# Kernel optimization log

Measured on AMD Instinct MI355X. Metric: run time of the kernel, lower is better.

## Reference

```python
import jax, jax.numpy as jnp
import numpy as np

B, T = 4, 8192
C = 64            # dilation_channels (also embedding size)
S = 256           # skip_dims
V = 256           # waveform_categories (8-bit mu-law)
CENTER = 128      # waveform_center_cat
DILATIONS = [1, 2, 4, 8, 16, 32, 64, 128, 256, 512] * 3  # 3 blocks, 30 layers
L = len(DILATIONS)


def setup_inputs() -> dict:
    key = jax.random.key(0)
    ks = jax.random.split(key, 16)
    waveform = jax.random.randint(ks[0], (B, T, 1), 0, V, dtype=jnp.int32)
    waveform_lens = jax.random.randint(ks[1], (B,), 0, T, dtype=jnp.int32)
    s = 0.05
    embed = jax.random.normal(ks[2], (V, C), dtype=jnp.float32) * s
    # conv_w[l, 0] applies to x[t-d], conv_w[l, 1] to x[t] (kernel_size=2)
    conv_w = jax.random.normal(ks[3], (L, 2, C, 2 * C), dtype=jnp.float32) * s
    conv_b = jnp.zeros((L, 2 * C), dtype=jnp.float32)
    res_w = jax.random.normal(ks[4], (L, C, C), dtype=jnp.float32) * s
    res_b = jnp.zeros((L, C), dtype=jnp.float32)
    skip_w = jax.random.normal(ks[5], (L, C, S), dtype=jnp.float32) * s
    skip_b = jnp.zeros((L, S), dtype=jnp.float32)
    w0 = jax.random.normal(ks[6], (S, V), dtype=jnp.float32) * s
    b0 = jnp.zeros((V,), dtype=jnp.float32)
    w1 = jax.random.normal(ks[7], (V, V), dtype=jnp.float32) * s
    b1 = jnp.zeros((V,), dtype=jnp.float32)
    return dict(waveform=waveform, waveform_lens=waveform_lens, embed=embed,
                conv_w=conv_w, conv_b=conv_b, res_w=res_w, res_b=res_b,
                skip_w=skip_w, skip_b=skip_b, w0=w0, b0=b0, w1=w1, b1=b1)


def _wavenet(wf, lens, embed, conv_w, conv_b, res_w, res_b, skip_w, skip_b, w0, b0, w1, b1):
    labels = wf[..., 0]                                          # (B, T) int
    # shift right with <go> = center category
    inp = jnp.concatenate(
        [jnp.full((B, 1), CENTER, dtype=labels.dtype), labels[:, :-1]], axis=1)
    x = embed[inp]                                               # (B, T, C)
    skip_sum = jnp.zeros((B, T, S), dtype=x.dtype)
    for i, d in enumerate(DILATIONS):
        # dilated causal conv, kernel 2: y[t] = x[t-d] @ W0 + x[t] @ W1 + b
        x_shift = jnp.pad(x, ((0, 0), (d, 0), (0, 0)))[:, :T]    # left pad d
        h = (jnp.einsum('btc,cf->btf', x_shift, conv_w[i, 0])
             + jnp.einsum('btc,cf->btf', x, conv_w[i, 1]) + conv_b[i])
        gate = jnp.tanh(h[..., :C]) * jax.nn.sigmoid(h[..., C:])  # (B, T, C)
        x = x + jnp.einsum('btc,cd->btd', gate, res_w[i]) + res_b[i]
        skip_sum = skip_sum + jnp.einsum('btc,cs->bts', gate, skip_w[i]) + skip_b[i]
    hid0 = jax.nn.relu(jnp.einsum('bts,sv->btv', skip_sum, w0) + b0)
    logits = jnp.einsum('btv,vu->btu', hid0, w1) + b1            # (B, T, V)
    logp = jax.nn.log_softmax(logits, axis=-1)
    ce = -jnp.take_along_axis(logp, labels[..., None], axis=-1)[..., 0]  # (B, T)
    mask = (jnp.arange(T)[None, :] < lens[:, None]).astype(logits.dtype)
    loss = jnp.sum(ce * mask) / jnp.maximum(jnp.sum(mask), 1.0)
    return loss


def reference(waveform, waveform_lens, embed, conv_w, conv_b, res_w, res_b,
              skip_w, skip_b, w0, b0, w1, b1):
    return _wavenet(waveform, waveform_lens, embed, conv_w, conv_b, res_w,
                    res_b, skip_w, skip_b, w0, b0, w1, b1)
```

## Files before the change

kernel.cpp:

```cpp
#include <hip/hip_runtime.h>

#define NB 4
#define NT 8192
#define NC 64
#define NS 256
#define NV 256
#define NL 30

typedef __attribute__((ext_vector_type(8))) short bf16x8;
typedef __attribute__((ext_vector_type(4))) float f32x4;
typedef unsigned short ushort_t;

#define MFMA(a, b, c) __builtin_amdgcn_mfma_f32_16x16x32_bf16(a, b, c, 0, 0, 0)

#define OFF_WCAT 0
#define SZ_WCAT  (NL * 16384)
#define OFF_RW   (OFF_WCAT + SZ_WCAT)
#define SZ_RW    (NL * 4096)
#define OFF_SWG  (OFF_RW + SZ_RW)
#define SZ_SWG   (6 * 81920)
#define OFF_W0   (OFF_SWG + SZ_SWG)
#define OFF_W1   (OFF_W0 + 65536)
#define TOTAL_W  (OFF_W1 + 65536)
#define N_PREP   (TOTAL_W + 1792)

#define X_ELEMS  (NB * NT * NC)
#define SK_ELEMS (NB * NT * NS)
#define G_ELEMS  (NB * NT * NC)

#define WS_SMALL ((size_t)(2 * X_ELEMS + SK_ELEMS + 5 * G_ELEMS + TOTAL_W) * 2 \
                  + 1792 * 4)
#define WS_BIG   ((size_t)(2 * X_ELEMS + 30 * G_ELEMS + TOTAL_W) * 2 + 1792 * 4)

__device__ inline ushort_t f2bu(float f) {
  union { float f; unsigned u; } v; v.f = f;
  unsigned r = v.u + 0x7FFFu + ((v.u >> 16) & 1u);
  return (ushort_t)(r >> 16);
}
__device__ inline float b2f(ushort_t h) {
  union { unsigned u; float f; } v; v.u = ((unsigned)h) << 16; return v.f;
}

__global__ void sentinel_kernel(float* __restrict__ out) {
  if (threadIdx.x == 0) out[0] = -1234.0f;
}

__global__ __launch_bounds__(256) void prep_kernel(
    const float* __restrict__ cw, const float* __restrict__ rw,
    const float* __restrict__ sw, const float* __restrict__ w0,
    const float* __restrict__ w1, const float* __restrict__ sb_all,
    ushort_t* __restrict__ wt, float* __restrict__ sbg,
    float* __restrict__ out0)
{
  int idx = blockIdx.x * 256 + threadIdx.x;
  if (idx == 0) out0[0] = 0.f;
  if (idx >= N_PREP) return;
  if (idx >= TOTAL_W) {
    int j = idx - TOTAL_W;
    if (j < 1536) {
      int g = j >> 8, n = j & 255;
      float s = 0.f;
#pragma unroll
      for (int jj = 0; jj < 5; ++jj) s += sb_all[(5 * g + jj) * 256 + n];
      sbg[j] = s;
    } else {
      int n = j - 1536;
      float s = 0.f;
      for (int jj = 0; jj < NL; ++jj) s += sb_all[jj * 256 + n];
      sbg[j] = s;
    }
    return;
  }
  float v;
  if (idx < OFF_RW) {
    int e = idx; int l = e >> 14; int r = e & 16383;
    int kk = r >> 12, n = (r >> 5) & 127, j = r & 31;
    int k = kk * 32 + j, tap = k >> 6, c = k & 63;
    v = cw[(((l * 2 + tap) << 6) + c) * 128 + n];
  } else if (idx < OFF_SWG) {
    int e = idx - OFF_RW; int l = e >> 12; int r = e & 4095;
    int kk = r >> 11, n = (r >> 5) & 63, j = r & 31;
    int k = kk * 32 + j;
    v = rw[((l << 6) + k) * 64 + n];
  } else if (idx < OFF_W0) {
    int e = idx - OFF_SWG; int g = e / 81920; int r = e % 81920;
    int kk = r >> 13; int rem = r & 8191;
    int n = rem >> 5, jj = rem & 31;
    int k = kk * 32 + jj;
    v = sw[(size_t)(320 * g + k) * 256 + n];
  } else if (idx < OFF_W1) {
    int e = idx - OFF_W0;
    int kk = e >> 13; int rem = e & 8191;
    int n = rem >> 5, jj = rem & 31;
    int k = kk * 32 + jj;
    v = w0[k * 256 + n];
  } else {
    int e = idx - OFF_W1;
    int kk = e >> 13; int rem = e & 8191;
    int n = rem >> 5, jj = rem & 31;
    int k = kk * 32 + jj;
    v = w1[k * 256 + n];
  }
  wt[idx] = f2bu(v);
}

__global__ __launch_bounds__(256) void embed_kernel(
    const int* __restrict__ wf, const float* __restrict__ embed,
    ushort_t* __restrict__ x0)
{
  const int bidx = blockIdx.x;
  const int bb = bidx >> 7;
  const int t0 = (bidx & 127) << 6;
  const int pos0 = bb * NT + t0;
  for (int e = threadIdx.x; e < 64 * 64; e += 256) {
    int p = e >> 6, c = e & 63;
    int t = t0 + p;
    int id = (t == 0) ? 128 : wf[bb * NT + t - 1];
    x0[(size_t)(pos0 + p) * NC + c] = f2bu(embed[id * NC + c]);
  }
}

__global__ __launch_bounds__(384) void chain5_kernel(
    const ushort_t* __restrict__ xin, ushort_t* __restrict__ xout,
    ushort_t* __restrict__ gates,
    const ushort_t* __restrict__ wt,
    const float* __restrict__ cb_all, const float* __restrict__ rb_all,
    int l0, const int* __restrict__ wf, const float* __restrict__ embf)
{
  __shared__ __align__(16) ushort_t xt[96][72];
  __shared__ __align__(16) ushort_t gt[96][72];

  const int tid = threadIdx.x;
  const int w = tid >> 6, lane = tid & 63;
  const int quad = lane >> 4, c16 = lane & 15;
  const int bb = blockIdx.x >> 7;
  const int t0 = (blockIdx.x & 127) << 6;
  const size_t row0 = (size_t)bb * NT;

#pragma unroll
  for (int i = 0; i < 2; ++i) {
    int e = tid + i * 384;
    int r = e >> 3, c0 = (e & 7) * 8;
    int t = t0 - 32 + r;
    bf16x8 v;
    if (t >= 0) {
      if (embf) {
        int id = (t == 0) ? 128 : wf[row0 + t - 1];
        const float* ep = embf + id * NC + c0;
#pragma unroll
        for (int jj = 0; jj < 8; ++jj) v[jj] = (short)f2bu(ep[jj]);
      } else {
        v = *(const bf16x8*)(xin + (row0 + t) * 64 + c0);
      }
    } else { bf16x8 z = {0, 0, 0, 0, 0, 0, 0, 0}; v = z; }
    *(bf16x8*)&xt[r][c0] = v;
  }
  __syncthreads();

  for (int j = 0; j < 5; ++j) {
    const int l = l0 + j;
    const int d = 1 << j;
    const ushort_t* wcat = wt + OFF_WCAT + l * 16384;
    const ushort_t* rww  = wt + OFF_RW + l * 4096;
    const float* cb = cb_all + l * 128;
    const float* rb = rb_all + l * 64;

    bf16x8 af[4];
    {
      int lr = w * 16 + c16;
#pragma unroll
      for (int kk = 0; kk < 4; ++kk) {
        int rr = (kk < 2) ? lr - d : lr;
        int ch = (kk & 1) * 32 + quad * 8;
        if (rr >= 0) af[kk] = *(const bf16x8*)&xt[rr][ch];
        else { bf16x8 z = {0, 0, 0, 0, 0, 0, 0, 0}; af[kk] = z; }
      }
    }
    __syncthreads();

    {
      f32x4 acc[8];
#pragma unroll
      for (int q = 0; q < 4; ++q) {
        float ba = cb[q * 16 + c16], bs = cb[q * 16 + c16 + 64];
        f32x4 va = {ba, ba, ba, ba}, vb = {bs, bs, bs, bs};
        acc[q] = va; acc[4 + q] = vb;
      }
#pragma unroll
      for (int kk = 0; kk < 4; ++kk) {
        const ushort_t* wp = wcat + kk * 4096 + c16 * 32 + quad * 8;
#pragma unroll
        for (int q = 0; q < 4; ++q) {
          acc[q]     = MFMA(af[kk], *(const bf16x8*)(wp + q * 512), acc[q]);
          acc[4 + q] = MFMA(af[kk], *(const bf16x8*)(wp + q * 512 + 2048), acc[4 + q]);
        }
      }
#pragma unroll
      for (int q = 0; q < 4; ++q)
#pragma unroll
        for (int r = 0; r < 4; ++r) {
          float e2 = __expf(2.f * acc[q][r]);
          float th = (e2 - 1.f) / (e2 + 1.f);
          float sg = 1.f / (1.f + __expf(-acc[4 + q][r]));
          gt[w * 16 + quad * 4 + r][q * 16 + c16] = f2bu(th * sg);
        }

      bf16x8 gf0 = *(const bf16x8*)&gt[w * 16 + c16][quad * 8];
      bf16x8 gf1 = *(const bf16x8*)&gt[w * 16 + c16][32 + quad * 8];

      f32x4 acc2[4];
#pragma unroll
      for (int q = 0; q < 4; ++q) {
        float bv = rb[q * 16 + c16];
        f32x4 z = {bv, bv, bv, bv};
        acc2[q] = z;
      }
      const ushort_t* wp2 = rww + c16 * 32 + quad * 8;
#pragma unroll
      for (int q = 0; q < 4; ++q)
        acc2[q] = MFMA(gf0, *(const bf16x8*)(wp2 + q * 512), acc2[q]);
#pragma unroll
      for (int q = 0; q < 4; ++q)
        acc2[q] = MFMA(gf1, *(const bf16x8*)(wp2 + q * 512 + 2048), acc2[q]);
#pragma unroll
      for (int q = 0; q < 4; ++q) {
        int n = q * 16 + c16;
#pragma unroll
        for (int r = 0; r < 4; ++r) {
          int rowi = w * 16 + quad * 4 + r;
          xt[rowi][n] = f2bu(b2f(xt[rowi][n]) + acc2[q][r]);
        }
      }
    }
    __syncthreads();

    {
      ushort_t* gslot = gates + (size_t)j * G_ELEMS;
      int e = tid;
      {
        int r = e >> 3, c0 = (e & 7) * 8;
        *(bf16x8*)(gslot + (row0 + t0 + r) * 64 + c0) =
            *(const bf16x8*)&gt[32 + r][c0];
      }
      e = tid + 384;
      if (e < 512) {
        int r = e >> 3, c0 = (e & 7) * 8;
        *(bf16x8*)(gslot + (row0 + t0 + r) * 64 + c0) =
            *(const bf16x8*)&gt[32 + r][c0];
      }
    }
  }
  __syncthreads();

  {
    int e = tid;
    {
      int r = e >> 3, c0 = (e & 7) * 8;
      *(bf16x8*)(xout + (row0 + t0 + r) * 64 + c0) = *(const bf16x8*)&xt[32 + r][c0];
    }
    e = tid + 384;
    if (e < 512) {
      int r = e >> 3, c0 = (e & 7) * 8;
      *(bf16x8*)(xout + (row0 + t0 + r) * 64 + c0) = *(const bf16x8*)&xt[32 + r][c0];
    }
  }
}

__global__ __launch_bounds__(384) void chain5hi_kernel(
    const ushort_t* __restrict__ xin, ushort_t* __restrict__ xout,
    ushort_t* __restrict__ gates,
    const ushort_t* __restrict__ wt,
    const float* __restrict__ cb_all, const float* __restrict__ rb_all,
    int lbase, int write_x)
{
  __shared__ __align__(16) ushort_t xt[96][72];
  __shared__ __align__(16) ushort_t gt[96][72];

  const int tid = threadIdx.x;
  const int w = tid >> 6, lane = tid & 63;
  const int quad = lane >> 4, c16 = lane & 15;
  const int bb = blockIdx.x >> 7;
  const int sub = blockIdx.x & 127;
  const int k = sub & 31;
  const int i0 = (sub >> 5) << 6;
  const size_t row0 = (size_t)bb * NT;

#pragma unroll
  for (int i = 0; i < 2; ++i) {
    int e = tid + i * 384;
    int r = e >> 3, c0 = (e & 7) * 8;
    int ii = i0 + r - 32;
    bf16x8 v;
    if (ii >= 0) v = *(const bf16x8*)(xin + (row0 + (size_t)ii * 32 + k) * 64 + c0);
    else { bf16x8 z = {0, 0, 0, 0, 0, 0, 0, 0}; v = z; }
    *(bf16x8*)&xt[r][c0] = v;
  }
  __syncthreads();

  for (int j = 0; j < 5; ++j) {
    const int l = lbase + j;
    const int d = 1 << j;
    const ushort_t* wcat = wt + OFF_WCAT + l * 16384;
    const ushort_t* rww  = wt + OFF_RW + l * 4096;
    const float* cb = cb_all + l * 128;
    const float* rb = rb_all + l * 64;

    bf16x8 af[4];
    {
      int lr = w * 16 + c16;
#pragma unroll
      for (int kk = 0; kk < 4; ++kk) {
        int rr = (kk < 2) ? lr - d : lr;
        int ch = (kk & 1) * 32 + quad * 8;
        if (rr >= 0) af[kk] = *(const bf16x8*)&xt[rr][ch];
        else { bf16x8 z = {0, 0, 0, 0, 0, 0, 0, 0}; af[kk] = z; }
      }
    }
    __syncthreads();

    {
      f32x4 acc[8];
#pragma unroll
      for (int q = 0; q < 4; ++q) {
        float ba = cb[q * 16 + c16], bs = cb[q * 16 + c16 + 64];
        f32x4 va = {ba, ba, ba, ba}, vb = {bs, bs, bs, bs};
        acc[q] = va; acc[4 + q] = vb;
      }
#pragma unroll
      for (int kk = 0; kk < 4; ++kk) {
        const ushort_t* wp = wcat + kk * 4096 + c16 * 32 + quad * 8;
#pragma unroll
        for (int q = 0; q < 4; ++q) {
          acc[q]     = MFMA(af[kk], *(const bf16x8*)(wp + q * 512), acc[q]);
          acc[4 + q] = MFMA(af[kk], *(const bf16x8*)(wp + q * 512 + 2048), acc[4 + q]);
        }
      }
#pragma unroll
      for (int q = 0; q < 4; ++q)
#pragma unroll
        for (int r = 0; r < 4; ++r) {
          float e2 = __expf(2.f * acc[q][r]);
          float th = (e2 - 1.f) / (e2 + 1.f);
          float sg = 1.f / (1.f + __expf(-acc[4 + q][r]));
          gt[w * 16 + quad * 4 + r][q * 16 + c16] = f2bu(th * sg);
        }

      if (write_x || j < 4) {
        bf16x8 gf0 = *(const bf16x8*)&gt[w * 16 + c16][quad * 8];
        bf16x8 gf1 = *(const bf16x8*)&gt[w * 16 + c16][32 + quad * 8];

        f32x4 acc2[4];
#pragma unroll
        for (int q = 0; q < 4; ++q) {
          float bv = rb[q * 16 + c16];
          f32x4 z = {bv, bv, bv, bv};
          acc2[q] = z;
        }
        const ushort_t* wp2 = rww + c16 * 32 + quad * 8;
#pragma unroll
        for (int q = 0; q < 4; ++q)
          acc2[q] = MFMA(gf0, *(const bf16x8*)(wp2 + q * 512), acc2[q]);
#pragma unroll
        for (int q = 0; q < 4; ++q)
          acc2[q] = MFMA(gf1, *(const bf16x8*)(wp2 + q * 512 + 2048), acc2[q]);
#pragma unroll
        for (int q = 0; q < 4; ++q) {
          int n = q * 16 + c16;
#pragma unroll
          for (int r = 0; r < 4; ++r) {
            int rowi = w * 16 + quad * 4 + r;
            xt[rowi][n] = f2bu(b2f(xt[rowi][n]) + acc2[q][r]);
          }
        }
      }
    }
    __syncthreads();

    {
      ushort_t* gslot = gates + (size_t)j * G_ELEMS;
      int e = tid;
      {
        int r = e >> 3, c0 = (e & 7) * 8;
        *(bf16x8*)(gslot + (row0 + (size_t)(i0 + r) * 32 + k) * 64 + c0) =
            *(const bf16x8*)&gt[32 + r][c0];
      }
      e = tid + 384;
      if (e < 512) {
        int r = e >> 3, c0 = (e & 7) * 8;
        *(bf16x8*)(gslot + (row0 + (size_t)(i0 + r) * 32 + k) * 64 + c0) =
            *(const bf16x8*)&gt[32 + r][c0];
      }
    }
  }
  __syncthreads();

  if (write_x) {
    int e = tid;
    {
      int r = e >> 3, c0 = (e & 7) * 8;
      *(bf16x8*)(xout + (row0 + (size_t)(i0 + r) * 32 + k) * 64 + c0) =
          *(const bf16x8*)&xt[32 + r][c0];
    }
    e = tid + 384;
    if (e < 512) {
      int r = e >> 3, c0 = (e & 7) * 8;
      *(bf16x8*)(xout + (row0 + (size_t)(i0 + r) * 32 + k) * 64 + c0) =
          *(const bf16x8*)&xt[32 + r][c0];
    }
  }
}

__global__ __launch_bounds__(256) void skip30_head_kernel(
    const ushort_t* __restrict__ gates,
    const ushort_t* __restrict__ wt,
    const float* __restrict__ sbtot,
    const float* __restrict__ b0, const float* __restrict__ b1,
    const int* __restrict__ wf, const int* __restrict__ lens,
    float* __restrict__ loss)
{
  __shared__ __align__(16) ushort_t wbuf[2][8192];
  __shared__ __align__(16) ushort_t tile[64][264];
  const int tid = threadIdx.x;
  const int w = tid >> 6, lane = tid & 63;
  const int quad = lane >> 4, c16 = lane & 15;
  const int bb = blockIdx.x >> 7;
  const int t0 = (blockIdx.x & 127) << 6;
  const int tb = t0 + w * 16;
  const size_t row0 = (size_t)bb * NT;
  const int mylen = lens[bb];
  const ushort_t* swg = wt + OFF_SWG;

  f32x4 acc[16];
#pragma unroll
  for (int nt = 0; nt < 16; ++nt) { f32x4 z = {0.f, 0.f, 0.f, 0.f}; acc[nt] = z; }

  const size_t arow = (row0 + tb + c16) * 64;
  bf16x8 wreg[4];
#pragma unroll
  for (int i = 0; i < 4; ++i)
    wreg[i] = ((const bf16x8*)swg)[tid + i * 256];
  bf16x8 af = *(const bf16x8*)(gates + arow + quad * 8);
  int cur = 0;

  for (int kk = 0; kk < 60; ++kk) {
#pragma unroll
    for (int i = 0; i < 4; ++i)
      ((bf16x8*)wbuf[cur])[tid + i * 256] = wreg[i];
    int kn = (kk + 1 < 60) ? kk + 1 : 59;
#pragma unroll
    for (int i = 0; i < 4; ++i)
      wreg[i] = ((const bf16x8*)(swg + (size_t)kn * 8192))[tid + i * 256];
    bf16x8 afn = *(const bf16x8*)(gates + (size_t)(kn >> 1) * G_ELEMS + arow +
                                  (kn & 1) * 32 + quad * 8);
    __syncthreads();
    const ushort_t* wp = wbuf[cur] + c16 * 32 + quad * 8;
#pragma unroll
    for (int nt = 0; nt < 16; ++nt)
      acc[nt] = MFMA(af, *(const bf16x8*)(wp + nt * 512), acc[nt]);
    af = afn; cur ^= 1;
  }

#pragma unroll
  for (int nt = 0; nt < 16; ++nt) {
    int n = nt * 16 + c16;
    float sbn = sbtot[n];
#pragma unroll
    for (int r = 0; r < 4; ++r)
      tile[w * 16 + quad * 4 + r][n] = f2bu(acc[nt][r] + sbn);
  }

  const ushort_t* w0T = wt + OFF_W0;
  f32x4 accA[16];
#pragma unroll
  for (int nt = 0; nt < 16; ++nt) {
    float bv = b0[nt * 16 + c16];
    f32x4 z = {bv, bv, bv, bv};
    accA[nt] = z;
  }
  for (int kk = 0; kk < 8; ++kk) {
#pragma unroll
    for (int i = 0; i < 4; ++i)
      ((bf16x8*)wbuf[0])[tid + i * 256] = ((const bf16x8*)(w0T + kk * 8192))[tid + i * 256];
    __syncthreads();
    bf16x8 hf = *(const bf16x8*)&tile[w * 16 + c16][kk * 32 + quad * 8];
    const ushort_t* wp = wbuf[0] + c16 * 32 + quad * 8;
#pragma unroll
    for (int nt = 0; nt < 16; ++nt)
      accA[nt] = MFMA(hf, *(const bf16x8*)(wp + nt * 512), accA[nt]);
    __syncthreads();
  }
#pragma unroll
  for (int nt = 0; nt < 16; ++nt)
#pragma unroll
    for (int r = 0; r < 4; ++r)
      tile[w * 16 + quad * 4 + r][nt * 16 + c16] = f2bu(fmaxf(accA[nt][r], 0.f));

  const ushort_t* w1T = wt + OFF_W1;
  f32x4 acc2[16];
#pragma unroll
  for (int nt = 0; nt < 16; ++nt) {
    float bv = b1[nt * 16 + c16];
    f32x4 z = {bv, bv, bv, bv};
    acc2[nt] = z;
  }
  for (int kk = 0; kk < 8; ++kk) {
#pragma unroll
    for (int i = 0; i < 4; ++i)
      ((bf16x8*)wbuf[0])[tid + i * 256] = ((const bf16x8*)(w1T + kk * 8192))[tid + i * 256];
    __syncthreads();
    bf16x8 hf = *(const bf16x8*)&tile[w * 16 + c16][kk * 32 + quad * 8];
    const ushort_t* wp = wbuf[0] + c16 * 32 + quad * 8;
#pragma unroll
    for (int nt = 0; nt < 16; ++nt)
      acc2[nt] = MFMA(hf, *(const bf16x8*)(wp + nt * 512), acc2[nt]);
    __syncthreads();
  }

  int lblv[4];
#pragma unroll
  for (int r = 0; r < 4; ++r)
    lblv[r] = wf[row0 + tb + quad * 4 + r];

  float local = 0.f;
#pragma unroll
  for (int r = 0; r < 4; ++r) {
    float m = -1e30f, tv = -1e30f;
#pragma unroll
    for (int nt = 0; nt < 16; ++nt) {
      float v = acc2[nt][r];
      m = fmaxf(m, v);
      if (lblv[r] == nt * 16 + c16) tv = v;
    }
#pragma unroll
    for (int dd = 1; dd < 16; dd <<= 1) m = fmaxf(m, __shfl_xor(m, dd));
    float s = 0.f;
#pragma unroll
    for (int nt = 0; nt < 16; ++nt) s += __expf(acc2[nt][r] - m);
#pragma unroll
    for (int dd = 1; dd < 16; dd <<= 1) {
      s += __shfl_xor(s, dd);
      tv = fmaxf(tv, __shfl_xor(tv, dd));
    }
    int t = tb + quad * 4 + r;
    if (c16 == 0 && t < mylen) local += (m + __logf(s)) - tv;
  }
#pragma unroll
  for (int dd = 1; dd < 64; dd <<= 1) local += __shfl_xor(local, dd);
  if (lane == 0 && local != 0.f) atomicAdd(loss, local);
}

__global__ __launch_bounds__(256) void skip_kernel(
    ushort_t* __restrict__ skip, const ushort_t* __restrict__ gates,
    const ushort_t* __restrict__ swg, const float* __restrict__ sbg,
    int first)
{
  __shared__ __align__(16) ushort_t wbuf[8192];
  const int tid = threadIdx.x;
  const int w = tid >> 6, lane = tid & 63;
  const int quad = lane >> 4, c16 = lane & 15;
  const int bb = blockIdx.x >> 7;
  const int t0 = (blockIdx.x & 127) << 6;
  const int tb = t0 + w * 16;
  const size_t row0 = (size_t)bb * NT;

  f32x4 acc[16];
#pragma unroll
  for (int nt = 0; nt < 16; ++nt) { f32x4 z = {0.f, 0.f, 0.f, 0.f}; acc[nt] = z; }

  const size_t arow = (row0 + tb + c16) * 64;
  for (int kk = 0; kk < 10; ++kk) {
#pragma unroll
    for (int i = 0; i < 4; ++i)
      ((bf16x8*)wbuf)[tid + i * 256] = ((const bf16x8*)(swg + kk * 8192))[tid + i * 256];
    __syncthreads();

    int slot = kk >> 1;
    bf16x8 af = *(const bf16x8*)(gates + (size_t)slot * G_ELEMS + arow +
                                 (kk & 1) * 32 + quad * 8);
    const ushort_t* wp = wbuf + c16 * 32 + quad * 8;
#pragma unroll
    for (int nt = 0; nt < 16; ++nt)
      acc[nt] = MFMA(af, *(const bf16x8*)(wp + nt * 512), acc[nt]);
    __syncthreads();
  }

#pragma unroll
  for (int nt = 0; nt < 16; ++nt) {
    int n = nt * 16 + c16;
    float sbn = sbg[n];
#pragma unroll
    for (int r = 0; r < 4; ++r) {
      size_t idx = (row0 + tb + quad * 4 + r) * 256 + n;
      float old = first ? 0.f : b2f(skip[idx]);
      skip[idx] = f2bu(old + acc[nt][r] + sbn);
    }
  }
}

__global__ __launch_bounds__(256) void head_kernel(
    const ushort_t* __restrict__ skip,
    const ushort_t* __restrict__ w0T, const float* __restrict__ b0,
    const ushort_t* __restrict__ w1T, const float* __restrict__ b1,
    const int* __restrict__ wf, const int* __restrict__ lens,
    float* __restrict__ loss)
{
  __shared__ __align__(16) ushort_t wbuf[8192];
  __shared__ __align__(16) ushort_t tile[64][264];
  const int tid = threadIdx.x;
  const int w = tid >> 6, lane = tid & 63;
  const int quad = lane >> 4, c16 = lane & 15;
  const int bb = blockIdx.x >> 7;
  const int t0 = (blockIdx.x & 127) << 6;
  const int tb = t0 + w * 16;
  const size_t row0 = (size_t)bb * NT;
  const int mylen = lens[bb];

#pragma unroll
  for (int i = 0; i < 8; ++i) {
    int e = lane + i * 64;
    int r = e >> 5, c0 = (e & 31) * 8;
    *(bf16x8*)&tile[w * 16 + r][c0] =
        *(const bf16x8*)(skip + (row0 + t0 + w * 16 + r) * 256 + c0);
  }

  f32x4 accA[16];
#pragma unroll
  for (int nt = 0; nt < 16; ++nt) {
    float bv = b0[nt * 16 + c16];
    f32x4 z = {bv, bv, bv, bv};
    accA[nt] = z;
  }
  for (int kk = 0; kk < 8; ++kk) {
#pragma unroll
    for (int i = 0; i < 4; ++i)
      ((bf16x8*)wbuf)[tid + i * 256] = ((const bf16x8*)(w0T + kk * 8192))[tid + i * 256];
    __syncthreads();
    bf16x8 af = *(const bf16x8*)&tile[w * 16 + c16][kk * 32 + quad * 8];
    const ushort_t* wp = wbuf + c16 * 32 + quad * 8;
#pragma unroll
    for (int nt = 0; nt < 16; ++nt)
      accA[nt] = MFMA(af, *(const bf16x8*)(wp + nt * 512), accA[nt]);
    __syncthreads();
  }
#pragma unroll
  for (int nt = 0; nt < 16; ++nt)
#pragma unroll
    for (int r = 0; r < 4; ++r)
      tile[w * 16 + quad * 4 + r][nt * 16 + c16] = f2bu(fmaxf(accA[nt][r], 0.f));

  f32x4 acc2[16];
#pragma unroll
  for (int nt = 0; nt < 16; ++nt) {
    float bv = b1[nt * 16 + c16];
    f32x4 z = {bv, bv, bv, bv};
    acc2[nt] = z;
  }
  for (int kk = 0; kk < 8; ++kk) {
#pragma unroll
    for (int i = 0; i < 4; ++i)
      ((bf16x8*)wbuf)[tid + i * 256] = ((const bf16x8*)(w1T + kk * 8192))[tid + i * 256];
    __syncthreads();
    bf16x8 hf = *(const bf16x8*)&tile[w * 16 + c16][kk * 32 + quad * 8];
    const ushort_t* wp = wbuf + c16 * 32 + quad * 8;
#pragma unroll
    for (int nt = 0; nt < 16; ++nt)
      acc2[nt] = MFMA(hf, *(const bf16x8*)(wp + nt * 512), acc2[nt]);
    __syncthreads();
  }

  int lblv[4];
#pragma unroll
  for (int r = 0; r < 4; ++r)
    lblv[r] = wf[row0 + tb + quad * 4 + r];

  float local = 0.f;
#pragma unroll
  for (int r = 0; r < 4; ++r) {
    float m = -1e30f, tv = -1e30f;
#pragma unroll
    for (int nt = 0; nt < 16; ++nt) {
      float v = acc2[nt][r];
      m = fmaxf(m, v);
      if (lblv[r] == nt * 16 + c16) tv = v;
    }
#pragma unroll
    for (int dd = 1; dd < 16; dd <<= 1) m = fmaxf(m, __shfl_xor(m, dd));
    float s = 0.f;
#pragma unroll
    for (int nt = 0; nt < 16; ++nt) s += __expf(acc2[nt][r] - m);
#pragma unroll
    for (int dd = 1; dd < 16; dd <<= 1) {
      s += __shfl_xor(s, dd);
      tv = fmaxf(tv, __shfl_xor(tv, dd));
    }
    int t = tb + quad * 4 + r;
    if (c16 == 0 && t < mylen) local += (m + __logf(s)) - tv;
  }
#pragma unroll
  for (int dd = 1; dd < 64; dd <<= 1) local += __shfl_xor(local, dd);
  if (lane == 0 && local != 0.f) atomicAdd(loss, local);
}

__global__ void finalize_kernel(const int* __restrict__ lens,
                                float* __restrict__ out)
{
  if (threadIdx.x == 0) {
    float den = 0.f;
    for (int b = 0; b < NB; ++b) {
      int l = lens[b];
      if (l > NT) l = NT;
      den += (float)l;
    }
    out[0] = out[0] / fmaxf(den, 1.f);
  }
}

extern "C" void kernel_launch(void* const* d_in, const int* in_sizes, int n_in,
                              void* d_out, int out_size, void* d_ws, size_t ws_size,
                              hipStream_t stream) {
  const int*   wf     = (const int*)d_in[0];
  const int*   lens   = (const int*)d_in[1];
  const float* embed  = (const float*)d_in[2];
  const float* conv_w = (const float*)d_in[3];
  const float* conv_b = (const float*)d_in[4];
  const float* res_w  = (const float*)d_in[5];
  const float* res_b  = (const float*)d_in[6];
  const float* skip_w = (const float*)d_in[7];
  const float* skip_b = (const float*)d_in[8];
  const float* w0     = (const float*)d_in[9];
  const float* b0     = (const float*)d_in[10];
  const float* w1     = (const float*)d_in[11];
  const float* b1     = (const float*)d_in[12];

  float* out = (float*)d_out;
  if (ws_size < WS_SMALL) {
    sentinel_kernel<<<1, 64, 0, stream>>>(out);
    return;
  }
  const bool big = (ws_size >= WS_BIG);

  if (big) {
    ushort_t* x0    = (ushort_t*)d_ws;
    ushort_t* x1    = x0 + X_ELEMS;
    ushort_t* gates = x1 + X_ELEMS;
    ushort_t* wt    = gates + 30 * (size_t)G_ELEMS;
    float*    sbg   = (float*)(wt + TOTAL_W);

    prep_kernel<<<(N_PREP + 255) / 256, 256, 0, stream>>>(
        conv_w, res_w, skip_w, w0, w1, skip_b, wt, sbg, out);

    const ushort_t* xin = x0;
    ushort_t* xout = x1;
    for (int blk = 0; blk < 3; ++blk) {
      const int l0 = blk * 10;
      chain5_kernel<<<512, 384, 0, stream>>>(
          xin, xout, gates + (size_t)(2 * blk) * 5 * G_ELEMS,
          wt, conv_b, res_b, l0, wf, blk == 0 ? embed : nullptr);
      { const ushort_t* t = xout; xout = (ushort_t*)xin; xin = t; }
      chain5hi_kernel<<<512, 384, 0, stream>>>(
          xin, xout, gates + (size_t)(2 * blk + 1) * 5 * G_ELEMS,
          wt, conv_b, res_b, l0 + 5, blk < 2 ? 1 : 0);
      { const ushort_t* t = xout; xout = (ushort_t*)xin; xin = t; }
    }

    skip30_head_kernel<<<512, 256, 0, stream>>>(
        gates, wt, sbg + 1536, b0, b1, wf, lens, out);
    finalize_kernel<<<1, 64, 0, stream>>>(lens, out);
  } else {
    ushort_t* x0    = (ushort_t*)d_ws;
    ushort_t* x1    = x0 + X_ELEMS;
    ushort_t* skip  = x1 + X_ELEMS;
    ushort_t* gates = skip + SK_ELEMS;
    ushort_t* wt    = gates + 5 * (size_t)G_ELEMS;
    float*    sbg   = (float*)(wt + TOTAL_W);

    prep_kernel<<<(N_PREP + 255) / 256, 256, 0, stream>>>(
        conv_w, res_w, skip_w, w0, w1, skip_b, wt, sbg, out);
    embed_kernel<<<512, 256, 0, stream>>>(wf, embed, x0);

    const ushort_t* xin = x0;
    ushort_t* xout = x1;
    for (int blk = 0; blk < 3; ++blk) {
      const int l0 = blk * 10;
      chain5_kernel<<<512, 384, 0, stream>>>(
          xin, xout, gates, wt, conv_b, res_b, l0, wf, nullptr);
      { const ushort_t* t = xout; xout = (ushort_t*)xin; xin = t; }
      skip_kernel<<<512, 256, 0, stream>>>(
          skip, gates, wt + OFF_SWG + (size_t)(2 * blk) * 81920,
          sbg + (size_t)(2 * blk) * 256, blk == 0 ? 1 : 0);
      chain5hi_kernel<<<512, 384, 0, stream>>>(
          xin, xout, gates, wt, conv_b, res_b, l0 + 5, blk < 2 ? 1 : 0);
      { const ushort_t* t = xout; xout = (ushort_t*)xin; xin = t; }
      skip_kernel<<<512, 256, 0, stream>>>(
          skip, gates, wt + OFF_SWG + (size_t)(2 * blk + 1) * 81920,
          sbg + (size_t)(2 * blk + 1) * 256, 0);
    }

    head_kernel<<<512, 256, 0, stream>>>(
        skip, wt + OFF_W0, b0, wt + OFF_W1, b1, wf, lens, out);
    finalize_kernel<<<1, 64, 0, stream>>>(lens, out);
  }
}
```

Baseline: 426.4 us.

## Replace fused high-dilation chain kernel with per-layer launches

For the last five layers of each dilation block (dilations 32 to 512), the fused chain5hi kernel is replaced by five separate layer_kernel launches. Each launch handles one 64-timestep tile per block, stages the concat conv weights in LDS, computes the gated activation, and applies the residual update. The aim is to avoid the halo recomputation and large shared tiles the fused kernel needs at large dilations, and to gain occupancy. The cost is more kernel launches and a global-memory round trip of x between layers.

```diff
diff --git a/kernel.cpp b/kernel.cpp
--- a/kernel.cpp
+++ b/kernel.cpp
@@ -266,6 +266,94 @@
   }
 }
 
+__global__ __launch_bounds__(256, 4) void layer_kernel(
+    const ushort_t* __restrict__ xin, ushort_t* __restrict__ xout,
+    ushort_t* __restrict__ gate_out,
+    const ushort_t* __restrict__ wcat_s, const float* __restrict__ cb,
+    const ushort_t* __restrict__ rww,    const float* __restrict__ rb,
+    int d, int write_res)
+{
+  __shared__ __align__(16) ushort_t lwc[16384];
+  __shared__ __align__(16) ushort_t gt[64][72];
+
+  const int tid = threadIdx.x;
+  const int w = tid >> 6, lane = tid & 63;
+  const int quad = lane >> 4, c16 = lane & 15;
+  const int bb = blockIdx.x >> 7;
+  const int t0 = (blockIdx.x & 127) << 6;
+  const int tb = t0 + w * 16;
+  const size_t row0 = (size_t)bb * NT;
+
+  {
+    bf16x8* dst = (bf16x8*)lwc;
+    const bf16x8* s1 = (const bf16x8*)wcat_s;
+#pragma unroll
+    for (int i = 0; i < 8; ++i) dst[tid + i * 256] = s1[tid + i * 256];
+  }
+
+  const int tA = tb + c16;
+  bf16x8 af[4];
+#pragma unroll
+  for (int kk = 0; kk < 4; ++kk) {
+    int ts = (kk < 2) ? (tA - d) : tA;
+    int ch = (kk & 1) * 32 + quad * 8;
+    if (ts >= 0) {
+      af[kk] = *(const bf16x8*)(xin + (row0 + ts) * 64 + ch);
+    } else {
+      bf16x8 z = {0, 0, 0, 0, 0, 0, 0, 0};
+      af[kk] = z;
+    }
+  }
+  __syncthreads();
+
+#pragma unroll
+  for (int q = 0; q < 4; ++q) {
+    int na = q * 16 + c16;
+    int nb2 = na + 64;
+    float ba = cb[na], bs = cb[nb2];
+    f32x4 va = {ba, ba, ba, ba}, vb = {bs, bs, bs, bs};
+#pragma unroll
+    for (int kk = 0; kk < 4; ++kk) {
+      va = MFMA(af[kk], *(const bf16x8*)&lwc[kk * 4096 + na * 32 + quad * 8], va);
+      vb = MFMA(af[kk], *(const bf16x8*)&lwc[kk * 4096 + nb2 * 32 + quad * 8], vb);
+    }
+#pragma unroll
+    for (int r = 0; r < 4; ++r) {
+      float e2 = __expf(2.f * va[r]);
+      float th = (e2 - 1.f) / (e2 + 1.f);
+      float sg = 1.f / (1.f + __expf(-vb[r]));
+      gt[w * 16 + quad * 4 + r][q * 16 + c16] = f2bu(th * sg);
+    }
+  }
+
+  bf16x8 gf0 = *(const bf16x8*)&gt[w * 16 + c16][quad * 8];
+  bf16x8 gf1 = *(const bf16x8*)&gt[w * 16 + c16][32 + quad * 8];
+
+  if (write_res) {
+    const ushort_t* wp2 = rww + c16 * 32 + quad * 8;
+#pragma unroll
+    for (int q = 0; q < 4; ++q) {
+      int n = q * 16 + c16;
+      float bv = rb[n];
+      f32x4 acc = {bv, bv, bv, bv};
+      acc = MFMA(gf0, *(const bf16x8*)(wp2 + q * 512), acc);
+      acc = MFMA(gf1, *(const bf16x8*)(wp2 + q * 512 + 2048), acc);
+#pragma unroll
+      for (int r = 0; r < 4; ++r) {
+        size_t idx = (row0 + tb + quad * 4 + r) * 64 + n;
+        xout[idx] = f2bu(b2f(xin[idx]) + acc[r]);
+      }
+    }
+  }
+
+#pragma unroll
+  for (int i = 0; i < 2; ++i) {
+    int e = lane + i * 64;
+    int rr = w * 16 + (e >> 3), c0 = (e & 7) * 8;
+    *(bf16x8*)(gate_out + (row0 + t0 + rr) * 64 + c0) = *(const bf16x8*)&gt[rr][c0];
+  }
+}
+
 __global__ __launch_bounds__(384) void chain5hi_kernel(
     const ushort_t* __restrict__ xin, ushort_t* __restrict__ xout,
     ushort_t* __restrict__ gates,
@@ -739,6 +827,10 @@
   }
   const bool big = (ws_size >= WS_BIG);
 
+  static const int dil[NL] = {1, 2, 4, 8, 16, 32, 64, 128, 256, 512,
+                              1, 2, 4, 8, 16, 32, 64, 128, 256, 512,
+                              1, 2, 4, 8, 16, 32, 64, 128, 256, 512};
+
   if (big) {
     ushort_t* x0    = (ushort_t*)d_ws;
     ushort_t* x1    = x0 + X_ELEMS;
@@ -754,13 +846,17 @@
     for (int blk = 0; blk < 3; ++blk) {
       const int l0 = blk * 10;
       chain5_kernel<<<512, 384, 0, stream>>>(
-          xin, xout, gates + (size_t)(2 * blk) * 5 * G_ELEMS,
+          xin, xout, gates + (size_t)l0 * G_ELEMS,
           wt, conv_b, res_b, l0, wf, blk == 0 ? embed : nullptr);
       { const ushort_t* t = xout; xout = (ushort_t*)xin; xin = t; }
-      chain5hi_kernel<<<512, 384, 0, stream>>>(
-          xin, xout, gates + (size_t)(2 * blk + 1) * 5 * G_ELEMS,
-          wt, conv_b, res_b, l0 + 5, blk < 2 ? 1 : 0);
-      { const ushort_t* t = xout; xout = (ushort_t*)xin; xin = t; }
+      for (int l = l0 + 5; l < l0 + 10; ++l) {
+        layer_kernel<<<512, 256, 0, stream>>>(
+            xin, xout, gates + (size_t)l * G_ELEMS,
+            wt + OFF_WCAT + l * 16384, conv_b + l * 128,
+            wt + OFF_RW + l * 4096,    res_b + l * 64,
+            dil[l], l < NL - 1 ? 1 : 0);
+        { const ushort_t* t = xout; xout = (ushort_t*)xin; xin = t; }
+      }
     }
 
     skip30_head_kernel<<<512, 256, 0, stream>>>(
```

After: 416.3 us, median of 2. -2.4%, faster.
